# Performance work log

Measured on AMD Instinct MI355X. Metric: run time of the kernel, lower is better.

## Reference

```python
import jax, jax.numpy as jnp
import numpy as np

N = 50000      # total nodes
E = 800000     # edges (before self loops)
B = 512        # graphs in batch
NODE_F = 9
GLOB_F = 4
IN_F = 13
H = 4          # heads
C = 16         # per-head channels (64 // 4)
HID = 64
NEG_SLOPE = 0.2


def setup_inputs() -> dict:
    key = jax.random.key(0)
    ks = jax.random.split(key, 32)
    inp = {}
    inp["node_feats"] = jax.random.normal(ks[0], (N, NODE_F), jnp.float32)
    inp["x_global_features"] = jax.random.normal(ks[1], (B, GLOB_F), jnp.float32)
    inp["edge_index"] = jax.random.randint(ks[2], (2, E), 0, N, jnp.int32)
    inp["batch_idx"] = jnp.sort(jax.random.randint(ks[3], (N,), 0, B, jnp.int32))
    dims = [IN_F, HID, HID]
    k = 4
    for l in range(3):
        s = 1.0 / np.sqrt(dims[l])
        inp[f"W{l}"] = jax.random.normal(ks[k], (dims[l], H * C), jnp.float32) * s; k += 1
        inp[f"att_src{l}"] = jax.random.normal(ks[k], (H, C), jnp.float32) * 0.1; k += 1
        inp[f"att_dst{l}"] = jax.random.normal(ks[k], (H, C), jnp.float32) * 0.1; k += 1
        inp[f"b{l}"] = jnp.zeros((H * C,), jnp.float32)
    mlp_dims = [(64, 64), (64, 64), (64, 64), (64, 1)]
    for i, (a, o) in enumerate(mlp_dims):
        inp[f"mlp_W{i}"] = jax.random.normal(ks[k], (a, o), jnp.float32) * (1.0 / np.sqrt(a)); k += 1
        inp[f"mlp_b{i}"] = jnp.zeros((o,), jnp.float32)
    return inp


def _gat_conv(x, src, dst, W, a_src, a_dst, bias, n):
    # h: [n, H, C]
    h = (x @ W).reshape(n, H, C)
    alpha_src = jnp.sum(h * a_src, axis=-1)   # [n, H]
    alpha_dst = jnp.sum(h * a_dst, axis=-1)   # [n, H]
    e = alpha_src[src] + alpha_dst[dst]       # [E', H]
    e = jax.nn.leaky_relu(e, NEG_SLOPE)
    # softmax over incoming edges per destination node (self loops guarantee >=1 edge)
    m = jax.ops.segment_max(e, dst, num_segments=n)
    e = jnp.exp(e - m[dst])
    s = jax.ops.segment_sum(e, dst, num_segments=n)
    alpha = e / s[dst]                        # [E', H]
    out = jax.ops.segment_sum(h[src] * alpha[:, :, None], dst, num_segments=n)
    return out.reshape(n, H * C) + bias


def _forward(node_feats, x_global_features,
             W0, att_src0, att_dst0, b0,
             W1, att_src1, att_dst1, b1,
             W2, att_src2, att_dst2, b2,
             mlp_W0, mlp_b0, mlp_W1, mlp_b1, mlp_W2, mlp_b2, mlp_W3, mlp_b3,
             edge_index, batch_idx):
    n = node_feats.shape[0]
    # concat per-graph global features onto each node
    x = jnp.concatenate([node_feats, x_global_features[batch_idx]], axis=1)  # [N, 13]
    loops = jnp.arange(n, dtype=edge_index.dtype)
    src = jnp.concatenate([edge_index[0], loops])
    dst = jnp.concatenate([edge_index[1], loops])
    x = jax.nn.relu(_gat_conv(x, src, dst, W0, att_src0, att_dst0, b0, n))
    x = jax.nn.relu(_gat_conv(x, src, dst, W1, att_src1, att_dst1, b1, n))
    x = _gat_conv(x, src, dst, W2, att_src2, att_dst2, b2, n)  # no act on last layer
    # scatter_mean over graphs
    sums = jax.ops.segment_sum(x, batch_idx, num_segments=B)
    cnt = jax.ops.segment_sum(jnp.ones((n,), x.dtype), batch_idx, num_segments=B)
    pooled = sums / jnp.clip(cnt, 1.0)[:, None]               # [B, 64]
    h = jax.nn.relu(pooled @ mlp_W0 + mlp_b0)
    h = jax.nn.relu(h @ mlp_W1 + mlp_b1)
    h = jax.nn.relu(h @ mlp_W2 + mlp_b2)
    out = h @ mlp_W3 + mlp_b3                                  # [B, 1]
    return out.reshape(-1)                                     # flatten -> [B]


def reference(node_feats, x_global_features,
              W0, att_src0, att_dst0, b0,
              W1, att_src1, att_dst1, b1,
              W2, att_src2, att_dst2, b2,
              mlp_W0, mlp_b0, mlp_W1, mlp_b1, mlp_W2, mlp_b2, mlp_W3, mlp_b3,
              edge_index, batch_idx):
    return _forward(node_feats, x_global_features,
                    W0, att_src0, att_dst0, b0,
                    W1, att_src1, att_dst1, b1,
                    W2, att_src2, att_dst2, b2,
                    mlp_W0, mlp_b0, mlp_W1, mlp_b1, mlp_W2, mlp_b2, mlp_W3, mlp_b3,
                    edge_index, batch_idx)
```

## Files before the change

### kernel.cpp

```cpp
#include <hip/hip_runtime.h>

#define GAT_H 4
#define GAT_HC 64
#define NEG_SLOPE 0.2f
#define DB 128
#define NBMAX 512
#define CHUNK 4096
#define EPT 16

__device__ __forceinline__ float lrelu(float x) { return x >= 0.f ? x : NEG_SLOPE * x; }

template <int K, bool CONCAT>
__global__ __launch_bounds__(256) void gemm_attn(
    const float* __restrict__ x, const float* __restrict__ nf,
    const float* __restrict__ gf, const int* __restrict__ batch,
    const float* __restrict__ W,
    const float* __restrict__ att_s, const float* __restrict__ att_d,
    float* __restrict__ h, float* __restrict__ asrc, float* __restrict__ adst,
    int N, int nwaves)
{
    int lane = threadIdx.x & 63;
    int wid = blockIdx.x * 4 + __builtin_amdgcn_readfirstlane(threadIdx.x >> 6);

    float w[K];
    #pragma unroll
    for (int k = 0; k < K; ++k) w[k] = W[k * 64 + lane];
    float as_c = att_s[lane];
    float ad_c = att_d[lane];

    for (int row = wid; row < N; row += nwaves) {
        float acc = 0.f;
        if (CONCAT) {
            #pragma unroll
            for (int k = 0; k < 9; ++k) acc = fmaf(nf[row * 9 + k], w[k], acc);
            int b = batch[row];
            #pragma unroll
            for (int k = 0; k < 4; ++k) acc = fmaf(gf[b * 4 + k], w[9 + k], acc);
        } else {
            #pragma unroll
            for (int k = 0; k < K; ++k) acc = fmaf(x[(size_t)row * K + k], w[k], acc);
        }
        h[(size_t)row * 64 + lane] = acc;
        float vs = acc * as_c;
        float vd = acc * ad_c;
        #pragma unroll
        for (int off = 8; off; off >>= 1) { vs += __shfl_xor(vs, off); vd += __shfl_xor(vd, off); }
        if ((lane & 15) == 0) {
            asrc[row * GAT_H + (lane >> 4)] = vs;
            adst[row * GAT_H + (lane >> 4)] = vd;
        }
    }
}


__global__ __launch_bounds__(256) void hist_bins(const int* __restrict__ dst,
                                                 unsigned* __restrict__ bin_cnt, int E)
{
    __shared__ unsigned lh[NBMAX];
    int t = threadIdx.x;
    lh[t] = 0; lh[t + 256] = 0;
    __syncthreads();
    for (int e = blockIdx.x * 256 + t; e < E; e += gridDim.x * 256)
        atomicAdd(&lh[((unsigned)dst[e]) >> 7], 1u);
    __syncthreads();
    unsigned v = lh[t];       if (v) atomicAdd(&bin_cnt[t], v);
    v = lh[t + 256];          if (v) atomicAdd(&bin_cnt[t + 256], v);
}

__global__ __launch_bounds__(256) void scan_bins(const unsigned* __restrict__ bin_cnt,
                                                 unsigned* __restrict__ bin_base,
                                                 unsigned* __restrict__ bin_fill,
                                                 int* __restrict__ indptr,
                                                 int nb, int N, int E)
{
    __shared__ unsigned buf[NBMAX];
    int t = threadIdx.x;
    buf[t] = (t < nb) ? bin_cnt[t] : 0u;
    buf[t + 256] = (t + 256 < nb) ? bin_cnt[t + 256] : 0u;
    bin_fill[t] = 0; bin_fill[t + 256] = 0;
    __syncthreads();
    for (int off = 1; off < NBMAX; off <<= 1) {
        unsigned a = 0, b = 0;
        if (t >= off) a = buf[t - off];
        b = buf[t + 256 - off];
        __syncthreads();
        buf[t] += a; buf[t + 256] += b;
        __syncthreads();
    }
    if (t == 0) { bin_base[0] = 0; indptr[N] = E; }
    if (t < nb) bin_base[t + 1] = buf[t];
    if (t + 256 < nb) bin_base[t + 257] = buf[t + 256];
}

__global__ __launch_bounds__(256) void bin_scatter(const int* __restrict__ src,
                                                   const int* __restrict__ dst,
                                                   const unsigned* __restrict__ bin_base,
                                                   unsigned* __restrict__ bin_fill,
                                                   unsigned* __restrict__ binned, int E)
{
    __shared__ unsigned lh[NBMAX];
    __shared__ int goff[NBMAX];
    __shared__ unsigned sorted[CHUNK];
    int t = threadIdx.x;
    lh[t] = 0; lh[t + 256] = 0;
    __syncthreads();
    int e0 = blockIdx.x * CHUNK;

    unsigned pk[EPT]; int bn[EPT]; unsigned rk[EPT];
    #pragma unroll
    for (int i = 0; i < EPT; ++i) {
        int e = e0 + i * 256 + t;
        bn[i] = -1;
        if (e < E) {
            unsigned d = (unsigned)dst[e];
            pk[i] = (d << 16) | (unsigned)src[e];
            bn[i] = (int)(d >> 7);
            rk[i] = atomicAdd(&lh[bn[i]], 1u);
        }
    }
    __syncthreads();
    unsigned c0 = lh[t], c1 = lh[t + 256];
    for (int off = 1; off < NBMAX; off <<= 1) {
        unsigned a = 0, b = 0;
        if (t >= off) a = lh[t - off];
        b = lh[t + 256 - off];
        __syncthreads();
        lh[t] += a; lh[t + 256] += b;
        __syncthreads();
    }
    unsigned x0 = lh[t] - c0, x1 = lh[t + 256] - c1;
    if (c0) { unsigned g = atomicAdd(&bin_fill[t], c0);
              goff[t] = (int)(bin_base[t] + g) - (int)x0; }
    if (c1) { unsigned g = atomicAdd(&bin_fill[t + 256], c1);
              goff[t + 256] = (int)(bin_base[t + 256] + g) - (int)x1; }
    lh[t] = x0; lh[t + 256] = x1;
    __syncthreads();
    #pragma unroll
    for (int i = 0; i < EPT; ++i)
        if (bn[i] >= 0) sorted[lh[bn[i]] + rk[i]] = pk[i];
    __syncthreads();
    int T = min(CHUNK, E - e0);
    for (int j = t; j < T; j += 256) {
        unsigned p = sorted[j];
        binned[goff[p >> 23] + j] = p;
    }
}

__global__ __launch_bounds__(256) void bin_finalize(const unsigned* __restrict__ binned,
                                                    const unsigned* __restrict__ bin_base,
                                                    int* __restrict__ csr_src,
                                                    int* __restrict__ indptr, int N)
{
    __shared__ unsigned lh[DB];
    __shared__ unsigned fill[DB];
    int t = threadIdx.x, b = blockIdx.x;
    unsigned base = bin_base[b];
    unsigned cnt = bin_base[b + 1] - base;
    if (t < DB) lh[t] = 0;
    __syncthreads();
    for (unsigned i = t; i < cnt; i += 256)
        atomicAdd(&lh[(binned[base + i] >> 16) & (DB - 1)], 1u);
    __syncthreads();
    unsigned c0 = (t < DB) ? lh[t] : 0;
    for (int off = 1; off < DB; off <<= 1) {
        unsigned a = 0;
        if (t >= off && t < DB) a = lh[t - off];
        __syncthreads();
        if (t < DB) lh[t] += a;
        __syncthreads();
    }
    if (t < DB) {
        unsigned excl = lh[t] - c0;
        int d = b * DB + t;
        if (d < N) indptr[d] = (int)(base + excl);
        fill[t] = excl;
    }
    __syncthreads();
    for (unsigned i = t; i < cnt; i += 256) {
        unsigned p = binned[base + i];
        unsigned pos = atomicAdd(&fill[(p >> 16) & (DB - 1)], 1u);
        csr_src[base + pos] = (int)(p & 0xFFFFu);
    }
}

template <bool RELU>
__global__ __launch_bounds__(256) void aggregate(
    const float* __restrict__ h, const float* __restrict__ asrc,
    const float* __restrict__ adst, const int* __restrict__ indptr,
    const int* __restrict__ csr_src, const float* __restrict__ bias,
    float* __restrict__ xout, int N)
{
    int lane = threadIdx.x & 63;
    int node = blockIdx.x * 4 + __builtin_amdgcn_readfirstlane(threadIdx.x >> 6);
    if (node >= N) return;
    int beg = __builtin_amdgcn_readfirstlane(indptr[node]);
    int end = __builtin_amdgcn_readfirstlane(indptr[node + 1]);

    unsigned h16 = (unsigned)(lane >> 4);
    unsigned un = (unsigned)node;
    float adst_n = adst[un * 4u + h16];
    float p0 = __expf(lrelu(asrc[un * 4u + h16] + adst_n));
    float sacc = p0;
    float acc = h[un * 64u + (unsigned)lane] * p0;

    int e = beg;
    for (; e + 8 <= end; e += 8) {
        int s[8]; float a[8], hv[8];
        #pragma unroll
        for (int i = 0; i < 8; ++i) s[i] = csr_src[e + i];
        #pragma unroll
        for (int i = 0; i < 8; ++i) a[i] = asrc[(unsigned)s[i] * 4u + h16];
        #pragma unroll
        for (int i = 0; i < 8; ++i) hv[i] = h[(unsigned)s[i] * 64u + (unsigned)lane];
        #pragma unroll
        for (int i = 0; i < 8; ++i) {
            float p = __expf(lrelu(a[i] + adst_n));
            sacc += p;
            acc = fmaf(hv[i], p, acc);
        }
    }
    for (; e + 2 <= end; e += 2) {
        int s0 = csr_src[e], s1 = csr_src[e + 1];
        float a0 = asrc[(unsigned)s0 * 4u + h16];
        float a1 = asrc[(unsigned)s1 * 4u + h16];
        float h0 = h[(unsigned)s0 * 64u + (unsigned)lane];
        float h1 = h[(unsigned)s1 * 64u + (unsigned)lane];
        float pa = __expf(lrelu(a0 + adst_n));
        float pb = __expf(lrelu(a1 + adst_n));
        sacc += pa + pb;
        acc = fmaf(h0, pa, acc);
        acc = fmaf(h1, pb, acc);
    }
    if (e < end) {
        int s = csr_src[e];
        float p = __expf(lrelu(asrc[(unsigned)s * 4u + h16] + adst_n));
        sacc += p;
        acc = fmaf(h[(unsigned)s * 64u + (unsigned)lane], p, acc);
    }

    float o = acc / sacc + bias[lane];
    if (RELU) o = fmaxf(o, 0.f);
    xout[un * 64u + (unsigned)lane] = o;
}

__global__ void pool_mlp(const float* __restrict__ x, const int* __restrict__ batch, int N,
                         const float* __restrict__ W0, const float* __restrict__ b0,
                         const float* __restrict__ W1, const float* __restrict__ b1,
                         const float* __restrict__ W2, const float* __restrict__ b2,
                         const float* __restrict__ W3, const float* __restrict__ b3,
                         float* __restrict__ out)
{
    __shared__ int bounds[2];
    __shared__ float red[4][64];
    __shared__ float hb[64];
    int b = blockIdx.x, t = threadIdx.x;

    if (t < 2) {
        int target = b + t;
        int lo = 0, hi = N;
        while (lo < hi) {
            int mid = (lo + hi) >> 1;
            if (batch[mid] < target) lo = mid + 1; else hi = mid;
        }
        bounds[t] = lo;
    }
    __syncthreads();
    int beg = bounds[0], end = bounds[1];

    int c = t & 63, w = t >> 6;
    float sum = 0.f;
    for (int n = beg + w; n < end; n += 4) sum += x[(size_t)n * 64 + c];
    red[w][c] = sum;
    __syncthreads();
    if (t < 64) {
        float v = red[0][t] + red[1][t] + red[2][t] + red[3][t];
        float cb = fmaxf((float)(end - beg), 1.0f);
        hb[t] = v / cb;
    }
    __syncthreads();

    float v0 = 0.f;
    if (t < 64) {
        v0 = b0[t];
        for (int k = 0; k < 64; ++k) v0 = fmaf(hb[k], W0[k * 64 + t], v0);
        v0 = fmaxf(v0, 0.f);
    }
    __syncthreads(); if (t < 64) hb[t] = v0; __syncthreads();
    if (t < 64) {
        v0 = b1[t];
        for (int k = 0; k < 64; ++k) v0 = fmaf(hb[k], W1[k * 64 + t], v0);
        v0 = fmaxf(v0, 0.f);
    }
    __syncthreads(); if (t < 64) hb[t] = v0; __syncthreads();
    if (t < 64) {
        v0 = b2[t];
        for (int k = 0; k < 64; ++k) v0 = fmaf(hb[k], W2[k * 64 + t], v0);
        v0 = fmaxf(v0, 0.f);
    }
    __syncthreads(); if (t < 64) hb[t] = v0; __syncthreads();
    if (t < 64) {
        float r = hb[t] * W3[t];
        #pragma unroll
        for (int off = 32; off; off >>= 1) r += __shfl_xor(r, off);
        if (t == 0) out[b] = r + b3[0];
    }
}

extern "C" void kernel_launch(void* const* d_in, const int* in_sizes, int n_in,
                              void* d_out, int out_size, void* d_ws, size_t ws_size,
                              hipStream_t stream)
{
    const float* node_feats = (const float*)d_in[0];
    const float* glob       = (const float*)d_in[1];
    const int*   edge_index = (const int*)d_in[2];
    const int*   batch      = (const int*)d_in[3];
    const float* W[3]  = {(const float*)d_in[4],  (const float*)d_in[8],  (const float*)d_in[12]};
    const float* As[3] = {(const float*)d_in[5],  (const float*)d_in[9],  (const float*)d_in[13]};
    const float* Ad[3] = {(const float*)d_in[6],  (const float*)d_in[10], (const float*)d_in[14]};
    const float* Bi[3] = {(const float*)d_in[7],  (const float*)d_in[11], (const float*)d_in[15]};
    const float* mW0 = (const float*)d_in[16]; const float* mb0 = (const float*)d_in[17];
    const float* mW1 = (const float*)d_in[18]; const float* mb1 = (const float*)d_in[19];
    const float* mW2 = (const float*)d_in[20]; const float* mb2 = (const float*)d_in[21];
    const float* mW3 = (const float*)d_in[22]; const float* mb3 = (const float*)d_in[23];
    float* out = (float*)d_out;

    int N = in_sizes[0] / 9;
    int E = in_sizes[2] / 2;
    int B = in_sizes[1] / 4;
    const int* esrc = edge_index;
    const int* edst = edge_index + E;
    int nb = (N + DB - 1) / DB;

    char* ws = (char*)d_ws;
    size_t off = 0;
    auto alloc = [&](size_t bytes) -> void* {
        void* p = ws + off;
        off = (off + bytes + 255) & ~(size_t)255;
        return p;
    };
    float*    xa       = (float*)alloc((size_t)N * 64 * 4);
    float*    xb       = (float*)alloc((size_t)N * 64 * 4);
    float*    hbuf     = (float*)alloc((size_t)N * 64 * 4);
    float*    asrc     = (float*)alloc((size_t)N * GAT_H * 4);
    float*    adst     = (float*)alloc((size_t)N * GAT_H * 4);
    int*      indptr   = (int*)alloc((size_t)(N + 1) * 4);
    int*      csr_src  = (int*)alloc((size_t)E * 4);
    unsigned* binned   = (unsigned*)alloc((size_t)E * 4);
    unsigned* bin_cnt  = (unsigned*)alloc(NBMAX * 4);
    unsigned* bin_base = (unsigned*)alloc((NBMAX + 1) * 4);
    unsigned* bin_fill = (unsigned*)alloc(NBMAX * 4);
    (void)ws_size;

    hipMemsetAsync(bin_cnt, 0, NBMAX * 4, stream);

    hist_bins<<<400, 256, 0, stream>>>(edst, bin_cnt, E);
    scan_bins<<<1, 256, 0, stream>>>(bin_cnt, bin_base, bin_fill, indptr, nb, N, E);
    bin_scatter<<<(E + CHUNK - 1) / CHUNK, 256, 0, stream>>>(esrc, edst, bin_base, bin_fill,
                                                             binned, E);
    bin_finalize<<<nb, 256, 0, stream>>>(binned, bin_base, csr_src, indptr, N);

    int gemmBlocks = 1024;
    int gemmWaves = gemmBlocks * 4;
    int grid4 = (N + 3) / 4;
    gemm_attn<13, true><<<gemmBlocks, 256, 0, stream>>>(nullptr, node_feats, glob, batch,
                                                        W[0], As[0], Ad[0], hbuf, asrc, adst,
                                                        N, gemmWaves);
    aggregate<true><<<grid4, 256, 0, stream>>>(hbuf, asrc, adst, indptr, csr_src, Bi[0], xb, N);
    gemm_attn<64, false><<<gemmBlocks, 256, 0, stream>>>(xb, nullptr, nullptr, nullptr,
                                                         W[1], As[1], Ad[1], hbuf, asrc, adst,
                                                         N, gemmWaves);
    aggregate<true><<<grid4, 256, 0, stream>>>(hbuf, asrc, adst, indptr, csr_src, Bi[1], xa, N);
    gemm_attn<64, false><<<gemmBlocks, 256, 0, stream>>>(xa, nullptr, nullptr, nullptr,
                                                         W[2], As[2], Ad[2], hbuf, asrc, adst,
                                                         N, gemmWaves);
    aggregate<false><<<grid4, 256, 0, stream>>>(hbuf, asrc, adst, indptr, csr_src, Bi[2], xb, N);

    pool_mlp<<<B, 256, 0, stream>>>(xb, batch, N,
                                    mW0, mb0, mW1, mb1, mW2, mb2, mW3, mb3, out);
}
```

Measured before the change: 206.9 us.

## Fuse GAT aggregation with next layer's linear transform and attention scores

```diff
diff --git a/kernel.cpp b/kernel.cpp
--- a/kernel.cpp
+++ b/kernel.cpp
@@ -10,11 +10,10 @@
 
 __device__ __forceinline__ float lrelu(float x) { return x >= 0.f ? x : NEG_SLOPE * x; }
 
-template <int K, bool CONCAT>
-__global__ __launch_bounds__(256) void gemm_attn(
-    const float* __restrict__ x, const float* __restrict__ nf,
-    const float* __restrict__ gf, const int* __restrict__ batch,
-    const float* __restrict__ W,
+template <int K>
+__global__ __launch_bounds__(256) void gemm0_attn(
+    const float* __restrict__ nf, const float* __restrict__ gf,
+    const int* __restrict__ batch, const float* __restrict__ W,
     const float* __restrict__ att_s, const float* __restrict__ att_d,
     float* __restrict__ h, float* __restrict__ asrc, float* __restrict__ adst,
     int N, int nwaves)
@@ -30,17 +29,13 @@
 
     for (int row = wid; row < N; row += nwaves) {
         float acc = 0.f;
-        if (CONCAT) {
-            #pragma unroll
-            for (int k = 0; k < 9; ++k) acc = fmaf(nf[row * 9 + k], w[k], acc);
-            int b = batch[row];
-            #pragma unroll
-            for (int k = 0; k < 4; ++k) acc = fmaf(gf[b * 4 + k], w[9 + k], acc);
-        } else {
-            #pragma unroll
-            for (int k = 0; k < K; ++k) acc = fmaf(x[(size_t)row * K + k], w[k], acc);
-        }
-        h[(size_t)row * 64 + lane] = acc;
+        #pragma unroll
+        for (int k = 0; k < 9; ++k) acc = fmaf(nf[row * 9 + k], w[k], acc);
+        int b = batch[row];
+        #pragma unroll
+        for (int k = 0; k < 4; ++k) acc = fmaf(gf[b * 4 + k], w[9 + k], acc);
+
+        h[(unsigned)row * 64u + (unsigned)lane] = acc;
         float vs = acc * as_c;
         float vd = acc * ad_c;
         #pragma unroll
@@ -183,64 +178,149 @@
     }
 }
 
-template <bool RELU>
-__global__ __launch_bounds__(256) void aggregate(
-    const float* __restrict__ h, const float* __restrict__ asrc,
-    const float* __restrict__ adst, const int* __restrict__ indptr,
+__global__ __launch_bounds__(256) void agg_gemm(
+    const float* __restrict__ hin, const float* __restrict__ asrcin,
+    const float* __restrict__ adstin, const int* __restrict__ indptr,
     const int* __restrict__ csr_src, const float* __restrict__ bias,
-    float* __restrict__ xout, int N)
+    const float* __restrict__ Wn, const float* __restrict__ attsn,
+    const float* __restrict__ attdn,
+    float* __restrict__ hout, float* __restrict__ asrcout, float* __restrict__ adstout,
+    int N, int nwaves)
+{
+    __shared__ float Wl[64 * 64];
+    int t = threadIdx.x;
+    for (int i = t; i < 64 * 64; i += 256) Wl[i] = Wn[i];
+    __syncthreads();
+
+    int lane = t & 63;
+    int wid = blockIdx.x * 4 + __builtin_amdgcn_readfirstlane(t >> 6);
+    unsigned h16 = (unsigned)(lane >> 4);
+    float bias_c = bias[lane];
+    float as_c = attsn[lane];
+    float ad_c = attdn[lane];
+
+    for (int node = wid; node < N; node += nwaves) {
+        int beg = __builtin_amdgcn_readfirstlane(indptr[node]);
+        int end = __builtin_amdgcn_readfirstlane(indptr[node + 1]);
+        unsigned un = (unsigned)node;
+
+        float adst_n = adstin[un * 4u + h16];
+        float p0 = __expf(lrelu(asrcin[un * 4u + h16] + adst_n));
+        float sacc = p0;
+        float acc = hin[un * 64u + (unsigned)lane] * p0;
+
+        int e = beg;
+        for (; e + 8 <= end; e += 8) {
+            int s[8]; float a[8], hv[8];
+            #pragma unroll
+            for (int i = 0; i < 8; ++i) s[i] = csr_src[e + i];
+            #pragma unroll
+            for (int i = 0; i < 8; ++i) a[i] = asrcin[(unsigned)s[i] * 4u + h16];
+            #pragma unroll
+            for (int i = 0; i < 8; ++i) hv[i] = hin[(unsigned)s[i] * 64u + (unsigned)lane];
+            #pragma unroll
+            for (int i = 0; i < 8; ++i) {
+                float p = __expf(lrelu(a[i] + adst_n));
+                sacc += p;
+                acc = fmaf(hv[i], p, acc);
+            }
+        }
+        for (; e + 2 <= end; e += 2) {
+            int s0 = csr_src[e], s1 = csr_src[e + 1];
+            float a0 = asrcin[(unsigned)s0 * 4u + h16];
+            float a1 = asrcin[(unsigned)s1 * 4u + h16];
+            float h0 = hin[(unsigned)s0 * 64u + (unsigned)lane];
+            float h1 = hin[(unsigned)s1 * 64u + (unsigned)lane];
+            float pa = __expf(lrelu(a0 + adst_n));
+            float pb = __expf(lrelu(a1 + adst_n));
+            sacc += pa + pb;
+            acc = fmaf(h0, pa, acc);
+            acc = fmaf(h1, pb, acc);
+        }
+        if (e < end) {
+            int s = csr_src[e];
+            float p = __expf(lrelu(asrcin[(unsigned)s * 4u + h16] + adst_n));
+            sacc += p;
+            acc = fmaf(hin[(unsigned)s * 64u + (unsigned)lane], p, acc);
+        }
+
+        float o = fmaxf(acc / sacc + bias_c, 0.f);
+
+        float acc2 = 0.f;
+        #pragma unroll
+        for (int k = 0; k < 64; ++k)
+            acc2 = fmaf(__shfl(o, k), Wl[k * 64 + lane], acc2);
+
+        hout[un * 64u + (unsigned)lane] = acc2;
+        float vs = acc2 * as_c;
+        float vd = acc2 * ad_c;
+        #pragma unroll
+        for (int off = 8; off; off >>= 1) { vs += __shfl_xor(vs, off); vd += __shfl_xor(vd, off); }
+        if ((lane & 15) == 0) {
+            asrcout[node * GAT_H + (lane >> 4)] = vs;
+            adstout[node * GAT_H + (lane >> 4)] = vd;
+        }
+    }
+}
+
+__global__ __launch_bounds__(256) void agg_final(
+    const float* __restrict__ hin, const float* __restrict__ asrcin,
+    const float* __restrict__ adstin, const int* __restrict__ indptr,
+    const int* __restrict__ csr_src, const float* __restrict__ bias,
+    float* __restrict__ xout, int N, int nwaves)
 {
     int lane = threadIdx.x & 63;
-    int node = blockIdx.x * 4 + __builtin_amdgcn_readfirstlane(threadIdx.x >> 6);
-    if (node >= N) return;
-    int beg = __builtin_amdgcn_readfirstlane(indptr[node]);
-    int end = __builtin_amdgcn_readfirstlane(indptr[node + 1]);
-
+    int wid = blockIdx.x * 4 + __builtin_amdgcn_readfirstlane(threadIdx.x >> 6);
     unsigned h16 = (unsigned)(lane >> 4);
-    unsigned un = (unsigned)node;
-    float adst_n = adst[un * 4u + h16];
-    float p0 = __expf(lrelu(asrc[un * 4u + h16] + adst_n));
-    float sacc = p0;
-    float acc = h[un * 64u + (unsigned)lane] * p0;
-
-    int e = beg;
-    for (; e + 8 <= end; e += 8) {
-        int s[8]; float a[8], hv[8];
-        #pragma unroll
-        for (int i = 0; i < 8; ++i) s[i] = csr_src[e + i];
-        #pragma unroll
-        for (int i = 0; i < 8; ++i) a[i] = asrc[(unsigned)s[i] * 4u + h16];
-        #pragma unroll
-        for (int i = 0; i < 8; ++i) hv[i] = h[(unsigned)s[i] * 64u + (unsigned)lane];
-        #pragma unroll
-        for (int i = 0; i < 8; ++i) {
-            float p = __expf(lrelu(a[i] + adst_n));
+    float bias_c = bias[lane];
+
+    for (int node = wid; node < N; node += nwaves) {
+        int beg = __builtin_amdgcn_readfirstlane(indptr[node]);
+        int end = __builtin_amdgcn_readfirstlane(indptr[node + 1]);
+        unsigned un = (unsigned)node;
+
+        float adst_n = adstin[un * 4u + h16];
+        float p0 = __expf(lrelu(asrcin[un * 4u + h16] + adst_n));
+        float sacc = p0;
+        float acc = hin[un * 64u + (unsigned)lane] * p0;
+
+        int e = beg;
+        for (; e + 8 <= end; e += 8) {
+            int s[8]; float a[8], hv[8];
+            #pragma unroll
+            for (int i = 0; i < 8; ++i) s[i] = csr_src[e + i];
+            #pragma unroll
+            for (int i = 0; i < 8; ++i) a[i] = asrcin[(unsigned)s[i] * 4u + h16];
+            #pragma unroll
+            for (int i = 0; i < 8; ++i) hv[i] = hin[(unsigned)s[i] * 64u + (unsigned)lane];
+            #pragma unroll
+            for (int i = 0; i < 8; ++i) {
+                float p = __expf(lrelu(a[i] + adst_n));
+                sacc += p;
+                acc = fmaf(hv[i], p, acc);
+            }
+        }
+        for (; e + 2 <= end; e += 2) {
+            int s0 = csr_src[e], s1 = csr_src[e + 1];
+            float a0 = asrcin[(unsigned)s0 * 4u + h16];
+            float a1 = asrcin[(unsigned)s1 * 4u + h16];
+            float h0 = hin[(unsigned)s0 * 64u + (unsigned)lane];
+            float h1 = hin[(unsigned)s1 * 64u + (unsigned)lane];
+            float pa = __expf(lrelu(a0 + adst_n));
+            float pb = __expf(lrelu(a1 + adst_n));
+            sacc += pa + pb;
+            acc = fmaf(h0, pa, acc);
+            acc = fmaf(h1, pb, acc);
+        }
+        if (e < end) {
+            int s = csr_src[e];
+            float p = __expf(lrelu(asrcin[(unsigned)s * 4u + h16] + adst_n));
             sacc += p;
-            acc = fmaf(hv[i], p, acc);
-        }
-    }
-    for (; e + 2 <= end; e += 2) {
-        int s0 = csr_src[e], s1 = csr_src[e + 1];
-        float a0 = asrc[(unsigned)s0 * 4u + h16];
-        float a1 = asrc[(unsigned)s1 * 4u + h16];
-        float h0 = h[(unsigned)s0 * 64u + (unsigned)lane];
-        float h1 = h[(unsigned)s1 * 64u + (unsigned)lane];
-        float pa = __expf(lrelu(a0 + adst_n));
-        float pb = __expf(lrelu(a1 + adst_n));
-        sacc += pa + pb;
-        acc = fmaf(h0, pa, acc);
-        acc = fmaf(h1, pb, acc);
-    }
-    if (e < end) {
-        int s = csr_src[e];
-        float p = __expf(lrelu(asrc[(unsigned)s * 4u + h16] + adst_n));
-        sacc += p;
-        acc = fmaf(h[(unsigned)s * 64u + (unsigned)lane], p, acc);
-    }
-
-    float o = acc / sacc + bias[lane];
-    if (RELU) o = fmaxf(o, 0.f);
-    xout[un * 64u + (unsigned)lane] = o;
+            acc = fmaf(hin[(unsigned)s * 64u + (unsigned)lane], p, acc);
+        }
+
+        xout[un * 64u + (unsigned)lane] = acc / sacc + bias_c;
+    }
 }
 
 __global__ void pool_mlp(const float* __restrict__ x, const int* __restrict__ batch, int N,
@@ -338,17 +418,19 @@
         off = (off + bytes + 255) & ~(size_t)255;
         return p;
     };
-    float*    xa       = (float*)alloc((size_t)N * 64 * 4);
-    float*    xb       = (float*)alloc((size_t)N * 64 * 4);
-    float*    hbuf     = (float*)alloc((size_t)N * 64 * 4);
-    float*    asrc     = (float*)alloc((size_t)N * GAT_H * 4);
-    float*    adst     = (float*)alloc((size_t)N * GAT_H * 4);
+    float*    hA       = (float*)alloc((size_t)N * 64 * 4);
+    float*    hB       = (float*)alloc((size_t)N * 64 * 4);
+    float*    asA      = (float*)alloc((size_t)N * GAT_H * 4);
+    float*    adA      = (float*)alloc((size_t)N * GAT_H * 4);
+    float*    asB      = (float*)alloc((size_t)N * GAT_H * 4);
+    float*    adB      = (float*)alloc((size_t)N * GAT_H * 4);
     int*      indptr   = (int*)alloc((size_t)(N + 1) * 4);
     int*      csr_src  = (int*)alloc((size_t)E * 4);
     unsigned* binned   = (unsigned*)alloc((size_t)E * 4);
     unsigned* bin_cnt  = (unsigned*)alloc(NBMAX * 4);
     unsigned* bin_base = (unsigned*)alloc((NBMAX + 1) * 4);
     unsigned* bin_fill = (unsigned*)alloc(NBMAX * 4);
+    float*    xfinal   = (float*)alloc((size_t)N * 64 * 4);
     (void)ws_size;
 
     hipMemsetAsync(bin_cnt, 0, NBMAX * 4, stream);
@@ -359,22 +441,27 @@
                                                              binned, E);
     bin_finalize<<<nb, 256, 0, stream>>>(binned, bin_base, csr_src, indptr, N);
 
-    int gemmBlocks = 1024;
-    int gemmWaves = gemmBlocks * 4;
-    int grid4 = (N + 3) / 4;
-    gemm_attn<13, true><<<gemmBlocks, 256, 0, stream>>>(nullptr, node_feats, glob, batch,
-                                                        W[0], As[0], Ad[0], hbuf, asrc, adst,
-                                                        N, gemmWaves);
-    aggregate<true><<<grid4, 256, 0, stream>>>(hbuf, asrc, adst, indptr, csr_src, Bi[0], xb, N);
-    gemm_attn<64, false><<<gemmBlocks, 256, 0, stream>>>(xb, nullptr, nullptr, nullptr,
-                                                         W[1], As[1], Ad[1], hbuf, asrc, adst,
-                                                         N, gemmWaves);
-    aggregate<true><<<grid4, 256, 0, stream>>>(hbuf, asrc, adst, indptr, csr_src, Bi[1], xa, N);
-    gemm_attn<64, false><<<gemmBlocks, 256, 0, stream>>>(xa, nullptr, nullptr, nullptr,
-                                                         W[2], As[2], Ad[2], hbuf, asrc, adst,
-                                                         N, gemmWaves);
-    aggregate<false><<<grid4, 256, 0, stream>>>(hbuf, asrc, adst, indptr, csr_src, Bi[2], xb, N);
-
-    pool_mlp<<<B, 256, 0, stream>>>(xb, batch, N,
+    gemm0_attn<13><<<1024, 256, 0, stream>>>(node_feats, glob, batch,
+                                             W[0], As[0], Ad[0], hA, asA, adA, N, 4096);
+
+    {
+        int blocks = 3125;
+        agg_gemm<<<blocks, 256, 0, stream>>>(hA, asA, adA, indptr, csr_src, Bi[0],
+                                             W[1], As[1], Ad[1], hB, asB, adB,
+                                             N, blocks * 4);
+    }
+    {
+        int blocks = 3125;
+        agg_gemm<<<blocks, 256, 0, stream>>>(hB, asB, adB, indptr, csr_src, Bi[1],
+                                             W[2], As[2], Ad[2], hA, asA, adA,
+                                             N, blocks * 4);
+    }
+    {
+        int blocks = 6250;
+        agg_final<<<blocks, 256, 0, stream>>>(hA, asA, adA, indptr, csr_src, Bi[2],
+                                              xfinal, N, blocks * 4);
+    }
+
+    pool_mlp<<<B, 256, 0, stream>>>(xfinal, batch, N,
                                     mW0, mb0, mW1, mb1, mW2, mb2, mW3, mb3, out);
 }
```

Result: slower. 236.8 us (+14.4%).

## Vectorize GAT aggregation with float4 loads and four edges per wavefront

Applied to the files above, without the earlier changes.

```diff
diff --git a/kernel.cpp b/kernel.cpp
--- a/kernel.cpp
+++ b/kernel.cpp
@@ -5,8 +5,8 @@
 #define NEG_SLOPE 0.2f
 #define DB 128
 #define NBMAX 512
-#define CHUNK 4096
-#define EPT 16
+#define CHUNK 2048
+#define EPT 8
 
 __device__ __forceinline__ float lrelu(float x) { return x >= 0.f ? x : NEG_SLOPE * x; }
 
@@ -40,7 +40,7 @@
             #pragma unroll
             for (int k = 0; k < K; ++k) acc = fmaf(x[(size_t)row * K + k], w[k], acc);
         }
-        h[(size_t)row * 64 + lane] = acc;
+        h[(unsigned)row * 64u + (unsigned)lane] = acc;
         float vs = acc * as_c;
         float vd = acc * ad_c;
         #pragma unroll
@@ -184,63 +184,101 @@
 }
 
 template <bool RELU>
-__global__ __launch_bounds__(256) void aggregate(
-    const float* __restrict__ h, const float* __restrict__ asrc,
-    const float* __restrict__ adst, const int* __restrict__ indptr,
+__global__ __launch_bounds__(256) void aggregate4(
+    const float* __restrict__ hin, const float* __restrict__ asrcin,
+    const float* __restrict__ adstin, const int* __restrict__ indptr,
     const int* __restrict__ csr_src, const float* __restrict__ bias,
-    float* __restrict__ xout, int N)
-{
-    int lane = threadIdx.x & 63;
-    int node = blockIdx.x * 4 + __builtin_amdgcn_readfirstlane(threadIdx.x >> 6);
-    if (node >= N) return;
-    int beg = __builtin_amdgcn_readfirstlane(indptr[node]);
-    int end = __builtin_amdgcn_readfirstlane(indptr[node + 1]);
-
-    unsigned h16 = (unsigned)(lane >> 4);
-    unsigned un = (unsigned)node;
-    float adst_n = adst[un * 4u + h16];
-    float p0 = __expf(lrelu(asrc[un * 4u + h16] + adst_n));
-    float sacc = p0;
-    float acc = h[un * 64u + (unsigned)lane] * p0;
-
-    int e = beg;
-    for (; e + 8 <= end; e += 8) {
-        int s[8]; float a[8], hv[8];
+    float* __restrict__ xout, int N, int nwaves)
+{
+    const float4* __restrict__ H4 = (const float4*)hin;
+    int t = threadIdx.x;
+    int lane = t & 63;
+    int slot = lane >> 4;
+    unsigned q = (unsigned)(lane & 15);
+    unsigned head = q >> 2;
+    int wid = blockIdx.x * 4 + __builtin_amdgcn_readfirstlane(t >> 6);
+
+    float4 bias_q = ((const float4*)bias)[q];
+
+    for (int node = wid; node < N; node += nwaves) {
+        int beg = __builtin_amdgcn_readfirstlane(indptr[node]);
+        int end = __builtin_amdgcn_readfirstlane(indptr[node + 1]);
+        unsigned un = (unsigned)node;
+
+        float adst_n = adstin[un * 4u + head];
+        float4 acc = make_float4(0.f, 0.f, 0.f, 0.f);
+        float sacc = 0.f;
+        if (slot == 0) {
+            float p0 = __expf(lrelu(asrcin[un * 4u + head] + adst_n));
+            float4 hv = H4[un * 16u + q];
+            acc.x = hv.x * p0; acc.y = hv.y * p0; acc.z = hv.z * p0; acc.w = hv.w * p0;
+            sacc = p0;
+        }
+
+        int e = beg;
+        for (; e + 16 <= end; e += 16) {
+            int s0 = csr_src[e + slot];
+            int s1 = csr_src[e + 4 + slot];
+            int s2 = csr_src[e + 8 + slot];
+            int s3 = csr_src[e + 12 + slot];
+            float a0 = asrcin[(unsigned)s0 * 4u + head];
+            float a1 = asrcin[(unsigned)s1 * 4u + head];
+            float a2 = asrcin[(unsigned)s2 * 4u + head];
+            float a3 = asrcin[(unsigned)s3 * 4u + head];
+            float4 v0 = H4[(unsigned)s0 * 16u + q];
+            float4 v1 = H4[(unsigned)s1 * 16u + q];
+            float4 v2 = H4[(unsigned)s2 * 16u + q];
+            float4 v3 = H4[(unsigned)s3 * 16u + q];
+            float p0 = __expf(lrelu(a0 + adst_n));
+            float p1 = __expf(lrelu(a1 + adst_n));
+            float p2 = __expf(lrelu(a2 + adst_n));
+            float p3 = __expf(lrelu(a3 + adst_n));
+            sacc += (p0 + p1) + (p2 + p3);
+            acc.x = fmaf(v0.x, p0, acc.x); acc.y = fmaf(v0.y, p0, acc.y);
+            acc.z = fmaf(v0.z, p0, acc.z); acc.w = fmaf(v0.w, p0, acc.w);
+            acc.x = fmaf(v1.x, p1, acc.x); acc.y = fmaf(v1.y, p1, acc.y);
+            acc.z = fmaf(v1.z, p1, acc.z); acc.w = fmaf(v1.w, p1, acc.w);
+            acc.x = fmaf(v2.x, p2, acc.x); acc.y = fmaf(v2.y, p2, acc.y);
+            acc.z = fmaf(v2.z, p2, acc.z); acc.w = fmaf(v2.w, p2, acc.w);
+            acc.x = fmaf(v3.x, p3, acc.x); acc.y = fmaf(v3.y, p3, acc.y);
+            acc.z = fmaf(v3.z, p3, acc.z); acc.w = fmaf(v3.w, p3, acc.w);
+        }
+        for (; e < end; e += 4) {
+            int idx = e + slot;
+            if (idx < end) {
+                int s = csr_src[idx];
+                float a = asrcin[(unsigned)s * 4u + head];
+                float4 hv = H4[(unsigned)s * 16u + q];
+                float p = __expf(lrelu(a + adst_n));
+                sacc += p;
+                acc.x = fmaf(hv.x, p, acc.x); acc.y = fmaf(hv.y, p, acc.y);
+                acc.z = fmaf(hv.z, p, acc.z); acc.w = fmaf(hv.w, p, acc.w);
+            }
+        }
+
         #pragma unroll
-        for (int i = 0; i < 8; ++i) s[i] = csr_src[e + i];
-        #pragma unroll
-        for (int i = 0; i < 8; ++i) a[i] = asrc[(unsigned)s[i] * 4u + h16];
-        #pragma unroll
-        for (int i = 0; i < 8; ++i) hv[i] = h[(unsigned)s[i] * 64u + (unsigned)lane];
-        #pragma unroll
-        for (int i = 0; i < 8; ++i) {
-            float p = __expf(lrelu(a[i] + adst_n));
-            sacc += p;
-            acc = fmaf(hv[i], p, acc);
-        }
-    }
-    for (; e + 2 <= end; e += 2) {
-        int s0 = csr_src[e], s1 = csr_src[e + 1];
-        float a0 = asrc[(unsigned)s0 * 4u + h16];
-        float a1 = asrc[(unsigned)s1 * 4u + h16];
-        float h0 = h[(unsigned)s0 * 64u + (unsigned)lane];
-        float h1 = h[(unsigned)s1 * 64u + (unsigned)lane];
-        float pa = __expf(lrelu(a0 + adst_n));
-        float pb = __expf(lrelu(a1 + adst_n));
-        sacc += pa + pb;
-        acc = fmaf(h0, pa, acc);
-        acc = fmaf(h1, pb, acc);
-    }
-    if (e < end) {
-        int s = csr_src[e];
-        float p = __expf(lrelu(asrc[(unsigned)s * 4u + h16] + adst_n));
-        sacc += p;
-        acc = fmaf(h[(unsigned)s * 64u + (unsigned)lane], p, acc);
-    }
-
-    float o = acc / sacc + bias[lane];
-    if (RELU) o = fmaxf(o, 0.f);
-    xout[un * 64u + (unsigned)lane] = o;
+        for (int off = 16; off <= 32; off <<= 1) {
+            acc.x += __shfl_xor(acc.x, off);
+            acc.y += __shfl_xor(acc.y, off);
+            acc.z += __shfl_xor(acc.z, off);
+            acc.w += __shfl_xor(acc.w, off);
+            sacc  += __shfl_xor(sacc,  off);
+        }
+
+        if (slot == 0) {
+            float inv = 1.0f / sacc;
+            float4 o;
+            o.x = fmaf(acc.x, inv, bias_q.x);
+            o.y = fmaf(acc.y, inv, bias_q.y);
+            o.z = fmaf(acc.z, inv, bias_q.z);
+            o.w = fmaf(acc.w, inv, bias_q.w);
+            if (RELU) {
+                o.x = fmaxf(o.x, 0.f); o.y = fmaxf(o.y, 0.f);
+                o.z = fmaxf(o.z, 0.f); o.w = fmaxf(o.w, 0.f);
+            }
+            ((float4*)xout)[un * 16u + q] = o;
+        }
+    }
 }
 
 __global__ void pool_mlp(const float* __restrict__ x, const int* __restrict__ batch, int N,
@@ -338,9 +376,8 @@
         off = (off + bytes + 255) & ~(size_t)255;
         return p;
     };
-    float*    xa       = (float*)alloc((size_t)N * 64 * 4);
-    float*    xb       = (float*)alloc((size_t)N * 64 * 4);
     float*    hbuf     = (float*)alloc((size_t)N * 64 * 4);
+    float*    xbuf     = (float*)alloc((size_t)N * 64 * 4);
     float*    asrc     = (float*)alloc((size_t)N * GAT_H * 4);
     float*    adst     = (float*)alloc((size_t)N * GAT_H * 4);
     int*      indptr   = (int*)alloc((size_t)(N + 1) * 4);
@@ -359,22 +396,24 @@
                                                              binned, E);
     bin_finalize<<<nb, 256, 0, stream>>>(binned, bin_base, csr_src, indptr, N);
 
-    int gemmBlocks = 1024;
-    int gemmWaves = gemmBlocks * 4;
-    int grid4 = (N + 3) / 4;
+    const int gemmBlocks = 1024;
+    const int aggBlocks = 6250;
     gemm_attn<13, true><<<gemmBlocks, 256, 0, stream>>>(nullptr, node_feats, glob, batch,
                                                         W[0], As[0], Ad[0], hbuf, asrc, adst,
-                                                        N, gemmWaves);
-    aggregate<true><<<grid4, 256, 0, stream>>>(hbuf, asrc, adst, indptr, csr_src, Bi[0], xb, N);
-    gemm_attn<64, false><<<gemmBlocks, 256, 0, stream>>>(xb, nullptr, nullptr, nullptr,
+                                                        N, gemmBlocks * 4);
+    aggregate4<true><<<aggBlocks, 256, 0, stream>>>(hbuf, asrc, adst, indptr, csr_src, Bi[0],
+                                                    xbuf, N, aggBlocks * 4);
+    gemm_attn<64, false><<<gemmBlocks, 256, 0, stream>>>(xbuf, nullptr, nullptr, nullptr,
                                                          W[1], As[1], Ad[1], hbuf, asrc, adst,
-                                                         N, gemmWaves);
-    aggregate<true><<<grid4, 256, 0, stream>>>(hbuf, asrc, adst, indptr, csr_src, Bi[1], xa, N);
-    gemm_attn<64, false><<<gemmBlocks, 256, 0, stream>>>(xa, nullptr, nullptr, nullptr,
+                                                         N, gemmBlocks * 4);
+    aggregate4<true><<<aggBlocks, 256, 0, stream>>>(hbuf, asrc, adst, indptr, csr_src, Bi[1],
+                                                    xbuf, N, aggBlocks * 4);
+    gemm_attn<64, false><<<gemmBlocks, 256, 0, stream>>>(xbuf, nullptr, nullptr, nullptr,
                                                          W[2], As[2], Ad[2], hbuf, asrc, adst,
-                                                         N, gemmWaves);
-    aggregate<false><<<grid4, 256, 0, stream>>>(hbuf, asrc, adst, indptr, csr_src, Bi[2], xb, N);
-
-    pool_mlp<<<B, 256, 0, stream>>>(xb, batch, N,
+                                                         N, gemmBlocks * 4);
+    aggregate4<false><<<aggBlocks, 256, 0, stream>>>(hbuf, asrc, adst, indptr, csr_src, Bi[2],
+                                                     xbuf, N, aggBlocks * 4);
+
+    pool_mlp<<<B, 256, 0, stream>>>(xbuf, batch, N,
                                     mW0, mb0, mW1, mb1, mW2, mb2, mW3, mb3, out);
 }
```

Measured after the change: 215.4 us. +4.1%, slower.
